# Optimization experiments

Hardware: AMD Instinct MI355X
Metric: run time of the kernel (lower is better)

Reference implementation:

```python
import jax, jax.numpy as jnp
import numpy as np

B, S, DIM, HEADS, DH = 1, 192, 512, 8, 64
LN_EPS = 1e-5


def setup_inputs() -> dict:
    key = jax.random.key(0)
    ks = jax.random.split(key, 5)
    rn = lambda k, shp: jax.random.normal(k, shp, dtype=jnp.float32) * 0.02
    return {
        "x": jax.random.normal(ks[0], (B, S, DIM), dtype=jnp.float32),
        "ln_w": jnp.ones((DIM,), jnp.float32),
        "ln_b": jnp.zeros((DIM,), jnp.float32),
        "W_abcde": rn(ks[1], (5 * HEADS * DH, DIM)),
        "b_abcde": jnp.zeros((5 * HEADS * DH,), jnp.float32),
        "W_K": rn(ks[2], (HEADS, DH, DH, DH)),
        "W_V": rn(ks[3], (HEADS, DH, DH, DH)),
        "W_out": rn(ks[4], (DIM, HEADS * DH)),
        "b_out": jnp.zeros((DIM,), jnp.float32),
    }


def reference(x, ln_w, ln_b, W_abcde, b_abcde, W_K, W_V, W_out, b_out):
    b, n, _ = x.shape
    # LayerNorm (biased variance, eps=1e-5, affine)
    mu = jnp.mean(x, axis=-1, keepdims=True)
    var = jnp.var(x, axis=-1, keepdims=True)
    xn = (x - mu) / jnp.sqrt(var + LN_EPS) * ln_w + ln_b
    # abcde projection, chunk into 5, split heads -> [b, n, h, d]
    proj = xn @ W_abcde.T + b_abcde
    a_, b_, c_, d_, e_ = [t.reshape(b, n, HEADS, DH) for t in jnp.split(proj, 5, axis=-1)]
    # cubic attention score chain (note: heads summed out in step2, reintroduced by a_)
    step1 = jnp.einsum('brnk,nijk->brij', c_, W_K)          # [b, r, d, d]
    step2 = jnp.einsum('brij,bqnj->briq', step1, b_)        # [b, r, d, q] (sum over heads of b_)
    attn = jnp.einsum('briq,bpni->bnpqr', step2, a_)        # [b, h, p, q, r]
    # "causal" mask: positions where p >= q set to 1e-6 (faithful to masked_fill_)
    t_idx = jnp.arange(n)[:, None, None]
    s_idx = jnp.arange(n)[None, :, None]
    mask = (t_idx >= s_idx)[None, None]                      # [1,1,p,q,1]
    attn = jnp.where(mask, jnp.float32(1e-6), attn)
    # 'b n p1 p2 p3 -> b n p3 (p1 p2)', scale by 1/dim_head, softmax over (p1 p2)
    attn = attn.transpose(0, 1, 4, 2, 3).reshape(b, HEADS, n, n * n) / DH
    attn = jax.nn.softmax(attn, axis=-1)
    # pairwise values: [b, p1, p2, h, d] -> 'b p s n h -> b n h (p s)'
    v = jnp.einsum('bpnh,bqng,nhgf->bpqnf', d_, e_, W_V)
    v = v.transpose(0, 3, 4, 1, 2).reshape(b, HEADS, DH, n * n)
    # weighted sum over pair axis, merge heads
    z = jnp.einsum('bnql,bnhl->bqnh', attn, v).reshape(b, n, HEADS * DH)
    return z @ W_out.T + b_out
```

## Files before the change

### kernel.cpp

```cpp
#include <hip/hip_runtime.h>
#include <hip/hip_bf16.h>
#include <cstdint>

#define SEQ 192

typedef float f32x4 __attribute__((ext_vector_type(4)));
typedef float f32x8 __attribute__((ext_vector_type(8)));
typedef __bf16 bf16;
typedef __bf16 bf16x8 __attribute__((ext_vector_type(8)));
typedef __bf16 bf16x4 __attribute__((ext_vector_type(4)));

#define MFMA_BF16(a, b, c) __builtin_amdgcn_mfma_f32_16x16x32_bf16(a, b, c, 0, 0, 0)

__device__ __forceinline__ bf16x8 cvt8(f32x8 v) {
  bf16x8 o;
#pragma unroll
  for (int i = 0; i < 8; i++) o[i] = (bf16)v[i];
  return o;
}

__global__ __launch_bounds__(256) void k1_prep(
    const float* __restrict__ x, const float* __restrict__ ln_w, const float* __restrict__ ln_b,
    const float* __restrict__ WV, bf16* __restrict__ xn_bf, bf16* __restrict__ WVt2) {
  int bid = blockIdx.x, tid = threadIdx.x;
  if (bid < 512) {
    int g = bid & 63, hh = bid >> 6;
    __shared__ float ld[64 * 65];
    int f = tid & 63, r4 = tid >> 6;
#pragma unroll
    for (int it = 0; it < 16; it++) {
      int hp = it * 4 + r4;
      ld[hp * 65 + f] = WV[(((size_t)(hh * 64 + hp) * 64 + g) * 64) + f];
    }
    __syncthreads();
    int hp2 = tid & 63;
#pragma unroll
    for (int it = 0; it < 16; it++) {
      int ff = it * 4 + r4;
      WVt2[(size_t)hh * 262144 + (size_t)(ff * 64 + g) * 64 + hp2] = (bf16)ld[hp2 * 65 + ff];
    }
    return;
  }
  bid -= 512;
  {
    int r = bid;
    const float* xr = x + (size_t)r * 512;
    float v0 = xr[tid], v1 = xr[tid + 256];
    float s = v0 + v1, s2 = v0 * v0 + v1 * v1;
#pragma unroll
    for (int off = 32; off > 0; off >>= 1) {
      s += __shfl_down(s, off);
      s2 += __shfl_down(s2, off);
    }
    __shared__ float redS[4], redS2[4];
    int wave = tid >> 6, lane = tid & 63;
    if (lane == 0) { redS[wave] = s; redS2[wave] = s2; }
    __syncthreads();
    float S = redS[0] + redS[1] + redS[2] + redS[3];
    float S2 = redS2[0] + redS2[1] + redS2[2] + redS2[3];
    float mean = S * (1.0f / 512.0f);
    float var = S2 * (1.0f / 512.0f) - mean * mean;
    float rstd = rsqrtf(var + 1e-5f);
    bf16* xnr = xn_bf + (size_t)r * 512;
    xnr[tid] = (bf16)((v0 - mean) * rstd * ln_w[tid] + ln_b[tid]);
    xnr[tid + 256] = (bf16)((v1 - mean) * rstd * ln_w[tid + 256] + ln_b[tid + 256]);
  }
}

template <int MODE>
__device__ __forceinline__ void gemm_body(const bf16* __restrict__ A, const bf16* __restrict__ Bt,
                                          bf16* __restrict__ C1, int N, int K,
                                          int nb, int mb, int tid) {
  int n0 = nb * 64, m0 = mb * 64;
  int wave = tid >> 6, lane = tid & 63;
  int lq = lane >> 4, l16 = lane & 15;
  const bf16* Ap = A + (size_t)(m0 + wave * 16 + l16) * K;
  f32x4 acc[4];
#pragma unroll
  for (int nt = 0; nt < 4; nt++) acc[nt] = (f32x4){0.f, 0.f, 0.f, 0.f};
  for (int k0 = 0; k0 < K; k0 += 32) {
    bf16x8 af = *(const bf16x8*)(Ap + k0 + lq * 8);
#pragma unroll
    for (int nt = 0; nt < 4; nt++) {
      bf16x8 bv = *(const bf16x8*)(Bt + (size_t)(n0 + nt * 16 + l16) * K + k0 + lq * 8);
      acc[nt] = MFMA_BF16(af, bv, acc[nt]);
    }
  }
  int cm = m0 + wave * 16 + lq * 4;
#pragma unroll
  for (int nt = 0; nt < 4; nt++) {
    int n = n0 + nt * 16 + l16;
    if constexpr (MODE == 1) {
#pragma unroll
      for (int rg = 0; rg < 4; rg++) C1[(size_t)(cm + rg) * N + n] = (bf16)acc[nt][rg];
    } else {
      int r = cm >> 6, i0 = cm & 63;
      bf16x4 pk = {(bf16)acc[nt][0], (bf16)acc[nt][1], (bf16)acc[nt][2], (bf16)acc[nt][3]};
      *(bf16x4*)(C1 + (size_t)r * 12288 + (size_t)n * 64 + i0) = pk;
    }
  }
}

__global__ __launch_bounds__(256) void k2_proj(
    const bf16* __restrict__ xn_bf, const float* __restrict__ Wab,
    const float* __restrict__ b_abcde, float* __restrict__ proj, bf16* __restrict__ a_bf,
    bf16* __restrict__ c_bf, bf16* __restrict__ d_bf) {
  int bid = blockIdx.x, tid = threadIdx.x;
  int nb = bid % 40, mb = bid / 40;
  int n0 = nb * 64, m0 = mb * 64;
  int wave = tid >> 6, lane = tid & 63;
  int lq = lane >> 4, l16 = lane & 15;
  const bf16* Ap = xn_bf + (size_t)(m0 + wave * 16 + l16) * 512;
  f32x4 acc[4];
#pragma unroll
  for (int nt = 0; nt < 4; nt++) acc[nt] = (f32x4){0.f, 0.f, 0.f, 0.f};
  for (int k0 = 0; k0 < 512; k0 += 32) {
    bf16x8 af = *(const bf16x8*)(Ap + k0 + lq * 8);
#pragma unroll
    for (int nt = 0; nt < 4; nt++) {
      f32x8 wv = *(const f32x8*)(Wab + (size_t)(n0 + nt * 16 + l16) * 512 + k0 + lq * 8);
      acc[nt] = MFMA_BF16(af, cvt8(wv), acc[nt]);
    }
  }
  int cm = m0 + wave * 16 + lq * 4;
#pragma unroll
  for (int nt = 0; nt < 4; nt++) {
    int n = n0 + nt * 16 + l16;
    int chunk = n >> 9, hcol = (n >> 6) & 7, i = n & 63;
#pragma unroll
    for (int rg = 0; rg < 4; rg++) {
      int m = cm + rg;
      float v = acc[nt][rg] + b_abcde[n];
      proj[(size_t)m * 2560 + n] = v;
      bf16 bv = (bf16)v;
      if (chunk == 0) a_bf[((size_t)hcol * SEQ + m) * 64 + i] = bv;
      else if (chunk == 2) c_bf[(size_t)m * 512 + (n - 1024)] = bv;
      else if (chunk == 3) d_bf[((size_t)hcol * SEQ + m) * 64 + i] = bv;
    }
  }
}

__global__ __launch_bounds__(256) void k3_mid(
    const bf16* __restrict__ c_bf, const float* __restrict__ WK, bf16* __restrict__ s1bf,
    const bf16* __restrict__ d_bf, const bf16* __restrict__ WVt2, bf16* __restrict__ tTt,
    const float* __restrict__ proj, bf16* __restrict__ eT_bf, float* __restrict__ ecum,
    bf16* __restrict__ bsum_bf) {
  __shared__ float el[64 * 65];
  int bid = blockIdx.x, tid = threadIdx.x;
  if (bid < 192) {
    int nb = bid % 64, mb = bid / 64;
    int n0 = nb * 64, m0 = mb * 64;
    int wave = tid >> 6, lane = tid & 63;
    int lq = lane >> 4, l16 = lane & 15;
    const bf16* Ap = c_bf + (size_t)(m0 + wave * 16 + l16) * 512;
    f32x4 acc[4];
#pragma unroll
    for (int nt = 0; nt < 4; nt++) acc[nt] = (f32x4){0.f, 0.f, 0.f, 0.f};
    size_t offn[4];
#pragma unroll
    for (int nt = 0; nt < 4; nt++) {
      int n = n0 + nt * 16 + l16;
      offn[nt] = (size_t)(n >> 6) * 4096 + (size_t)(n & 63) * 64;
    }
    for (int k0 = 0; k0 < 512; k0 += 32) {
      bf16x8 af = *(const bf16x8*)(Ap + k0 + lq * 8);
      size_t kb = (size_t)(k0 >> 6) * 262144 + (k0 & 32) + lq * 8;
#pragma unroll
      for (int nt = 0; nt < 4; nt++) {
        f32x8 wv = *(const f32x8*)(WK + kb + offn[nt]);
        acc[nt] = MFMA_BF16(af, cvt8(wv), acc[nt]);
      }
    }
    int cm = m0 + wave * 16 + lq * 4;
#pragma unroll
    for (int nt = 0; nt < 4; nt++) {
      int n = n0 + nt * 16 + l16;
#pragma unroll
      for (int rg = 0; rg < 4; rg++) s1bf[(size_t)(cm + rg) * 4096 + n] = (bf16)acc[nt][rg];
    }
    return;
  }
  bid -= 192;
  if (bid < 1536) {
    int h = bid / 192, rem = bid % 192;
    gemm_body<1>(d_bf + (size_t)h * 12288, WVt2 + (size_t)h * 262144,
                 tTt + (size_t)h * 786432, 4096, 64, rem % 64, rem / 64, tid);
    return;
  }
  bid -= 1536;
  if (bid < 8) {
    int h = bid;
    float carry = 0.f;
    for (int ch = 0; ch < 3; ch++) {
      int pbase = ch * 64;
      for (int idx = tid; idx < 4096; idx += 256) {
        int pl = idx >> 6, g = idx & 63;
        el[pl * 65 + g] = proj[(size_t)(pbase + pl) * 2560 + 2048 + h * 64 + g];
      }
      __syncthreads();
      for (int idx = tid; idx < 4096; idx += 256) {
        int g = idx >> 6, ql = idx & 63;
        eT_bf[((size_t)h * 64 + g) * SEQ + pbase + ql] = (bf16)el[ql * 65 + g];
      }
      if (tid < 64) {
        float run = carry;
        for (int pl = 0; pl < 64; pl++) {
          run += el[pl * 65 + tid];
          ecum[(size_t)h * 12288 + (pbase + pl) * 64 + tid] = run;
        }
        carry = run;
      }
      __syncthreads();
    }
    return;
  }
  bid -= 8;
  {
    int j = tid & 63, qg = tid >> 6;
#pragma unroll
    for (int qi = 0; qi < 16; qi++) {
      int q = bid * 64 + qg * 16 + qi;
      float s = 0.f;
#pragma unroll
      for (int hh = 0; hh < 8; hh++) s += proj[(size_t)q * 2560 + 512 + hh * 64 + j];
      bsum_bf[q * 64 + j] = (bf16)s;
    }
  }
}

__global__ __launch_bounds__(256) void k4_step2(const bf16* __restrict__ s1bf,
                                                const bf16* __restrict__ bsum_bf,
                                                bf16* __restrict__ s2bf) {
  int bid = blockIdx.x;
  gemm_body<2>(s1bf, bsum_bf, s2bf, 192, 64, bid % 3, bid / 3, threadIdx.x);
}

__global__ __launch_bounds__(256) void k5_attn(
    const bf16* __restrict__ a_bf, const bf16* __restrict__ s2bf,
    const bf16* __restrict__ eT_bf, const float* __restrict__ ecum,
    bf16* __restrict__ ew_bf, float* __restrict__ Lsum) {
  int r = blockIdx.x, h = blockIdx.y;
  int tid = threadIdx.x, wave = tid >> 6, lane = tid & 63;
  int lq = lane >> 4, l16 = lane & 15;
  __shared__ __align__(16) bf16 wch[4][16 * 40];
  __shared__ float redL[4];
  int pt[3] = {wave, wave + 4, 11 - wave};

  const bf16* ah = a_bf + (size_t)h * 12288;
  const bf16* s2r = s2bf + (size_t)r * 12288;
  const bf16* eh = eT_bf + (size_t)h * 12288;
  const float* ech = ecum + (size_t)h * 12288;
  bf16* myw = &wch[wave][0];

  bf16x8 afr[3][2];
#pragma unroll
  for (int mt = 0; mt < 3; mt++)
#pragma unroll
    for (int kc = 0; kc < 2; kc++)
      afr[mt][kc] = *(const bf16x8*)(ah + (pt[mt] * 16 + l16) * 64 + kc * 32 + lq * 8);

  f32x4 ewacc[3][4];
#pragma unroll
  for (int mt = 0; mt < 3; mt++)
#pragma unroll
    for (int nt = 0; nt < 4; nt++) ewacc[mt][nt] = (f32x4){0.f, 0.f, 0.f, 0.f};
  float lpart = 0.f;

  for (int c = 0; c < 6; c++) {
    if (c * 32 + 31 <= wave * 16) continue;
    bf16x8 efr[4];
#pragma unroll
    for (int nt = 0; nt < 4; nt++)
      efr[nt] = *(const bf16x8*)(eh + (nt * 16 + l16) * SEQ + c * 32 + lq * 8);
    bf16x8 bq0[2], bq1[2];
#pragma unroll
    for (int sub = 0; sub < 2; sub++) {
      int q = c * 32 + sub * 16 + l16;
      bq0[sub] = *(const bf16x8*)(s2r + q * 64 + lq * 8);
      bq1[sub] = *(const bf16x8*)(s2r + q * 64 + 32 + lq * 8);
    }
#pragma unroll
    for (int mt = 0; mt < 3; mt++) {
      int ptile = pt[mt];
      if (c * 32 + 31 <= ptile * 16) continue;
#pragma unroll
      for (int sub = 0; sub < 2; sub++) {
        if (c * 32 + sub * 16 + 15 <= ptile * 16) {
#pragma unroll
          for (int rg = 0; rg < 4; rg++) myw[(lq * 4 + rg) * 40 + sub * 16 + l16] = (bf16)0.f;
          continue;
        }
        f32x4 sv = (f32x4){0.f, 0.f, 0.f, 0.f};
        sv = MFMA_BF16(afr[mt][0], bq0[sub], sv);
        sv = MFMA_BF16(afr[mt][1], bq1[sub], sv);
        int q = c * 32 + sub * 16 + l16;
        int p0 = ptile * 16 + lq * 4;
#pragma unroll
        for (int rg = 0; rg < 4; rg++) {
          float wv = (q > p0 + rg) ? __expf(sv[rg] * 0.015625f) : 0.f;
          lpart += wv;
          myw[(lq * 4 + rg) * 40 + sub * 16 + l16] = (bf16)wv;
        }
      }
      bf16x8 wf = *(const bf16x8*)(myw + l16 * 40 + lq * 8);
#pragma unroll
      for (int nt = 0; nt < 4; nt++) ewacc[mt][nt] = MFMA_BF16(wf, efr[nt], ewacc[mt][nt]);
    }
  }

  bf16* ewout = ew_bf + ((size_t)h * SEQ + r) * 12288;
#pragma unroll
  for (int mt = 0; mt < 3; mt++)
#pragma unroll
    for (int nt = 0; nt < 4; nt++)
#pragma unroll
      for (int rg = 0; rg < 4; rg++) {
        int p = pt[mt] * 16 + lq * 4 + rg;
        int g = nt * 16 + l16;
        ewout[p * 64 + g] = (bf16)(ewacc[mt][nt][rg] + ech[p * 64 + g]);
      }

#pragma unroll
  for (int off = 32; off > 0; off >>= 1) lpart += __shfl_down(lpart, off);
  if (lane == 0) redL[wave] = lpart;
  __syncthreads();
  if (tid == 0) Lsum[h * SEQ + r] = redL[0] + redL[1] + redL[2] + redL[3];
}

__global__ __launch_bounds__(512) void k5b_z(
    const bf16* __restrict__ ew_bf, const bf16* __restrict__ tTt, float* __restrict__ Zpart) {
  int h = blockIdx.x, mt = blockIdx.y, ks = blockIdx.z;
  int tid = threadIdx.x, wave = tid >> 6, lane = tid & 63;
  int lq = lane >> 4, l16 = lane & 15;
  __shared__ float zred[8][16][66];
  const bf16* ewh = ew_bf + ((size_t)h * SEQ + mt * 16) * 12288;
  const bf16* th = tTt + (size_t)h * 786432;
  f32x4 acc[4];
#pragma unroll
  for (int nt = 0; nt < 4; nt++) acc[nt] = (f32x4){0.f, 0.f, 0.f, 0.f};
  for (int jj = 0; jj < 12; jj++) {
    int kc = ks * 96 + wave * 12 + jj;
    int p = kc >> 1, g0 = (kc & 1) * 32;
    bf16x8 af = *(const bf16x8*)(ewh + (size_t)l16 * 12288 + kc * 32 + lq * 8);
#pragma unroll
    for (int nt = 0; nt < 4; nt++) {
      bf16x8 tf = *(const bf16x8*)(th + (size_t)p * 4096 + (nt * 16 + l16) * 64 + g0 + lq * 8);
      acc[nt] = MFMA_BF16(af, tf, acc[nt]);
    }
  }
#pragma unroll
  for (int nt = 0; nt < 4; nt++)
#pragma unroll
    for (int rg = 0; rg < 4; rg++) zred[wave][lq * 4 + rg][nt * 16 + l16] = acc[nt][rg];
  __syncthreads();
#pragma unroll
  for (int o = 0; o < 2; o++) {
    int idx = o * 512 + tid;
    int rloc = idx >> 6, f = idx & 63;
    float s = 0.f;
#pragma unroll
    for (int wv = 0; wv < 8; wv++) s += zred[wv][rloc][f];
    Zpart[(size_t)ks * 98304 + (size_t)(mt * 16 + rloc) * 512 + h * 64 + f] = s;
  }
}

__global__ __launch_bounds__(256) void k6_out(
    const float* __restrict__ Zpart, const float* __restrict__ Lsum,
    const float* __restrict__ Wout, const float* __restrict__ b_out, float* __restrict__ out) {
  int bid = blockIdx.x, tid = threadIdx.x;
  int nb = bid & 7, mb = bid >> 3;
  int n0 = nb * 64, m0 = mb * 64;
  int wave = tid >> 6, lane = tid & 63;
  int lq = lane >> 4, l16 = lane & 15;
  int m = m0 + wave * 16 + l16;
  f32x4 acc[4];
#pragma unroll
  for (int nt = 0; nt < 4; nt++) acc[nt] = (f32x4){0.f, 0.f, 0.f, 0.f};
  for (int k0 = 0; k0 < 512; k0 += 32) {
    int h = k0 >> 6;
    float L = Lsum[h * SEQ + m] + 18528.0f;
    float rL = 1.0f / L;
    size_t zo = (size_t)m * 512 + k0 + lq * 8;
    f32x8 s = *(const f32x8*)(Zpart + zo);
    s += *(const f32x8*)(Zpart + 98304 + zo);
    s += *(const f32x8*)(Zpart + 196608 + zo);
    s += *(const f32x8*)(Zpart + 294912 + zo);
    bf16x8 af = cvt8(s * rL);
#pragma unroll
    for (int nt = 0; nt < 4; nt++) {
      f32x8 wv = *(const f32x8*)(Wout + (size_t)(n0 + nt * 16 + l16) * 512 + k0 + lq * 8);
      acc[nt] = MFMA_BF16(af, cvt8(wv), acc[nt]);
    }
  }
  int cm = m0 + wave * 16 + lq * 4;
#pragma unroll
  for (int nt = 0; nt < 4; nt++) {
    int n = n0 + nt * 16 + l16;
    float bv = b_out[n];
#pragma unroll
    for (int rg = 0; rg < 4; rg++) out[(size_t)(cm + rg) * 512 + n] = acc[nt][rg] + bv;
  }
}

static const size_t OFF_PROJ = 0;
static const size_t OFF_ECUM = 491520;
static const size_t OFF_XN = 589824;
static const size_t OFF_ZPART = 638976;
static const size_t OFF_LSUM = 1032192;
static const size_t OFF_WVT = 2473984;
static const size_t OFF_A = 3522560;
static const size_t OFF_C = 3571712;
static const size_t OFF_D = 3620864;
static const size_t OFF_ET = 3670016;
static const size_t OFF_BSUM = 3719168;
static const size_t OFF_S1 = 3725312;
static const size_t OFF_S2 = 4118528;
static const size_t OFF_TT = 5298176;
static const size_t OFF_EW = 8493056;

extern "C" void kernel_launch(void* const* d_in, const int* in_sizes, int n_in,
                              void* d_out, int out_size, void* d_ws, size_t ws_size,
                              hipStream_t stream) {
  (void)in_sizes; (void)n_in; (void)out_size; (void)ws_size;
  const float* x = (const float*)d_in[0];
  const float* ln_w = (const float*)d_in[1];
  const float* ln_b = (const float*)d_in[2];
  const float* W_abcde = (const float*)d_in[3];
  const float* b_abcde = (const float*)d_in[4];
  const float* W_K = (const float*)d_in[5];
  const float* W_V = (const float*)d_in[6];
  const float* W_out = (const float*)d_in[7];
  const float* b_out = (const float*)d_in[8];
  float* out = (float*)d_out;
  float* ws = (float*)d_ws;

  float* proj = ws + OFF_PROJ;
  float* ecum = ws + OFF_ECUM;
  bf16* xn_bf = (bf16*)(ws + OFF_XN);
  float* Zpart = ws + OFF_ZPART;
  float* Lsum = ws + OFF_LSUM;
  bf16* WVt2 = (bf16*)(ws + OFF_WVT);
  bf16* a_bf = (bf16*)(ws + OFF_A);
  bf16* c_bf = (bf16*)(ws + OFF_C);
  bf16* d_bf = (bf16*)(ws + OFF_D);
  bf16* eT_bf = (bf16*)(ws + OFF_ET);
  bf16* bsum_bf = (bf16*)(ws + OFF_BSUM);
  bf16* s1bf = (bf16*)(ws + OFF_S1);
  bf16* s2bf = (bf16*)(ws + OFF_S2);
  bf16* tTt = (bf16*)(ws + OFF_TT);
  bf16* ew_bf = (bf16*)(ws + OFF_EW);

  k1_prep<<<704, 256, 0, stream>>>(x, ln_w, ln_b, W_V, xn_bf, WVt2);
  k2_proj<<<120, 256, 0, stream>>>(xn_bf, W_abcde, b_abcde, proj, a_bf, c_bf, d_bf);
  k3_mid<<<1739, 256, 0, stream>>>(c_bf, W_K, s1bf, d_bf, WVt2, tTt, proj, eT_bf, ecum,
                                   bsum_bf);
  k4_step2<<<576, 256, 0, stream>>>(s1bf, bsum_bf, s2bf);
  k5_attn<<<dim3(SEQ, 8), 256, 0, stream>>>(a_bf, s2bf, eT_bf, ecum, ew_bf, Lsum);
  k5b_z<<<dim3(8, 12, 4), 512, 0, stream>>>(ew_bf, tTt, Zpart);
  k6_out<<<24, 256, 0, stream>>>(Zpart, Lsum, W_out, b_out, out);
}
```

Measured before the change: 255.5 us.

## Batch score MFMAs in attention kernel and retile Z reduction over more K splits

In k5_attn, all score MFMAs for the three p-tiles are now issued before the exp and LDS staging, and the per-wave staging buffer is split per tile and double-buffered by chunk parity. The goal is more independent MFMA work and fewer read-after-write stalls, paid for with more LDS and a launch bound of three blocks. k5b_z now computes two 16-row M tiles per block so each B fragment is reused twice, and the K split grows from 4 to 8 to keep the grid size the same. k6_out sums eight partials instead of four, and the Lsum offset moves to make room for the larger Zpart buffer.

```diff
diff --git a/kernel.cpp b/kernel.cpp
--- a/kernel.cpp
+++ b/kernel.cpp
@@ -235,14 +235,14 @@
   gemm_body<2>(s1bf, bsum_bf, s2bf, 192, 64, bid % 3, bid / 3, threadIdx.x);
 }
 
-__global__ __launch_bounds__(256) void k5_attn(
+__global__ __launch_bounds__(256, 3) void k5_attn(
     const bf16* __restrict__ a_bf, const bf16* __restrict__ s2bf,
     const bf16* __restrict__ eT_bf, const float* __restrict__ ecum,
     bf16* __restrict__ ew_bf, float* __restrict__ Lsum) {
   int r = blockIdx.x, h = blockIdx.y;
   int tid = threadIdx.x, wave = tid >> 6, lane = tid & 63;
   int lq = lane >> 4, l16 = lane & 15;
-  __shared__ __align__(16) bf16 wch[4][16 * 40];
+  __shared__ __align__(16) bf16 wch[2][4][3][16 * 40];
   __shared__ float redL[4];
   int pt[3] = {wave, wave + 4, 11 - wave};
 
@@ -250,7 +250,6 @@
   const bf16* s2r = s2bf + (size_t)r * 12288;
   const bf16* eh = eT_bf + (size_t)h * 12288;
   const float* ech = ecum + (size_t)h * 12288;
-  bf16* myw = &wch[wave][0];
 
   bf16x8 afr[3][2];
 #pragma unroll
@@ -268,41 +267,55 @@
 
   for (int c = 0; c < 6; c++) {
     if (c * 32 + 31 <= wave * 16) continue;
+    int par = c & 1;
     bf16x8 efr[4];
 #pragma unroll
     for (int nt = 0; nt < 4; nt++)
       efr[nt] = *(const bf16x8*)(eh + (nt * 16 + l16) * SEQ + c * 32 + lq * 8);
-    bf16x8 bq0[2], bq1[2];
+    bf16x8 bq[2][2];
 #pragma unroll
     for (int sub = 0; sub < 2; sub++) {
       int q = c * 32 + sub * 16 + l16;
-      bq0[sub] = *(const bf16x8*)(s2r + q * 64 + lq * 8);
-      bq1[sub] = *(const bf16x8*)(s2r + q * 64 + 32 + lq * 8);
-    }
+      bq[sub][0] = *(const bf16x8*)(s2r + q * 64 + lq * 8);
+      bq[sub][1] = *(const bf16x8*)(s2r + q * 64 + 32 + lq * 8);
+    }
+    f32x4 sacc[3][2];
 #pragma unroll
     for (int mt = 0; mt < 3; mt++) {
-      int ptile = pt[mt];
-      if (c * 32 + 31 <= ptile * 16) continue;
+      if (c * 32 + 31 <= pt[mt] * 16) continue;
 #pragma unroll
       for (int sub = 0; sub < 2; sub++) {
-        if (c * 32 + sub * 16 + 15 <= ptile * 16) {
-#pragma unroll
-          for (int rg = 0; rg < 4; rg++) myw[(lq * 4 + rg) * 40 + sub * 16 + l16] = (bf16)0.f;
+        if (c * 32 + sub * 16 + 15 <= pt[mt] * 16) continue;
+        f32x4 sv = (f32x4){0.f, 0.f, 0.f, 0.f};
+        sv = MFMA_BF16(afr[mt][0], bq[sub][0], sv);
+        sacc[mt][sub] = MFMA_BF16(afr[mt][1], bq[sub][1], sv);
+      }
+    }
+#pragma unroll
+    for (int mt = 0; mt < 3; mt++) {
+      if (c * 32 + 31 <= pt[mt] * 16) continue;
+      bf16* mybuf = &wch[par][wave][mt][0];
+#pragma unroll
+      for (int sub = 0; sub < 2; sub++) {
+        if (c * 32 + sub * 16 + 15 <= pt[mt] * 16) {
+#pragma unroll
+          for (int rg = 0; rg < 4; rg++) mybuf[(lq * 4 + rg) * 40 + sub * 16 + l16] = (bf16)0.f;
           continue;
         }
-        f32x4 sv = (f32x4){0.f, 0.f, 0.f, 0.f};
-        sv = MFMA_BF16(afr[mt][0], bq0[sub], sv);
-        sv = MFMA_BF16(afr[mt][1], bq1[sub], sv);
         int q = c * 32 + sub * 16 + l16;
-        int p0 = ptile * 16 + lq * 4;
+        int p0 = pt[mt] * 16 + lq * 4;
 #pragma unroll
         for (int rg = 0; rg < 4; rg++) {
-          float wv = (q > p0 + rg) ? __expf(sv[rg] * 0.015625f) : 0.f;
+          float wv = (q > p0 + rg) ? __expf(sacc[mt][sub][rg] * 0.015625f) : 0.f;
           lpart += wv;
-          myw[(lq * 4 + rg) * 40 + sub * 16 + l16] = (bf16)wv;
+          mybuf[(lq * 4 + rg) * 40 + sub * 16 + l16] = (bf16)wv;
         }
       }
-      bf16x8 wf = *(const bf16x8*)(myw + l16 * 40 + lq * 8);
+    }
+#pragma unroll
+    for (int mt = 0; mt < 3; mt++) {
+      if (c * 32 + 31 <= pt[mt] * 16) continue;
+      bf16x8 wf = *(const bf16x8*)(&wch[par][wave][mt][l16 * 40 + lq * 8]);
 #pragma unroll
       for (int nt = 0; nt < 4; nt++) ewacc[mt][nt] = MFMA_BF16(wf, efr[nt], ewacc[mt][nt]);
     }
@@ -333,34 +346,42 @@
   int tid = threadIdx.x, wave = tid >> 6, lane = tid & 63;
   int lq = lane >> 4, l16 = lane & 15;
   __shared__ float zred[8][16][66];
-  const bf16* ewh = ew_bf + ((size_t)h * SEQ + mt * 16) * 12288;
+  const bf16* ewh = ew_bf + ((size_t)h * SEQ + mt * 32) * 12288;
   const bf16* th = tTt + (size_t)h * 786432;
-  f32x4 acc[4];
-#pragma unroll
-  for (int nt = 0; nt < 4; nt++) acc[nt] = (f32x4){0.f, 0.f, 0.f, 0.f};
-  for (int jj = 0; jj < 12; jj++) {
-    int kc = ks * 96 + wave * 12 + jj;
+  f32x4 acc[2][4];
+#pragma unroll
+  for (int m2 = 0; m2 < 2; m2++)
+#pragma unroll
+    for (int nt = 0; nt < 4; nt++) acc[m2][nt] = (f32x4){0.f, 0.f, 0.f, 0.f};
+  for (int jj = 0; jj < 6; jj++) {
+    int kc = ks * 48 + wave * 6 + jj;
     int p = kc >> 1, g0 = (kc & 1) * 32;
-    bf16x8 af = *(const bf16x8*)(ewh + (size_t)l16 * 12288 + kc * 32 + lq * 8);
+    bf16x8 af0 = *(const bf16x8*)(ewh + (size_t)l16 * 12288 + kc * 32 + lq * 8);
+    bf16x8 af1 = *(const bf16x8*)(ewh + (size_t)(16 + l16) * 12288 + kc * 32 + lq * 8);
 #pragma unroll
     for (int nt = 0; nt < 4; nt++) {
       bf16x8 tf = *(const bf16x8*)(th + (size_t)p * 4096 + (nt * 16 + l16) * 64 + g0 + lq * 8);
-      acc[nt] = MFMA_BF16(af, tf, acc[nt]);
-    }
-  }
-#pragma unroll
-  for (int nt = 0; nt < 4; nt++)
-#pragma unroll
-    for (int rg = 0; rg < 4; rg++) zred[wave][lq * 4 + rg][nt * 16 + l16] = acc[nt][rg];
-  __syncthreads();
-#pragma unroll
-  for (int o = 0; o < 2; o++) {
-    int idx = o * 512 + tid;
-    int rloc = idx >> 6, f = idx & 63;
-    float s = 0.f;
-#pragma unroll
-    for (int wv = 0; wv < 8; wv++) s += zred[wv][rloc][f];
-    Zpart[(size_t)ks * 98304 + (size_t)(mt * 16 + rloc) * 512 + h * 64 + f] = s;
+      acc[0][nt] = MFMA_BF16(af0, tf, acc[0][nt]);
+      acc[1][nt] = MFMA_BF16(af1, tf, acc[1][nt]);
+    }
+  }
+#pragma unroll
+  for (int m2 = 0; m2 < 2; m2++) {
+    if (m2) __syncthreads();
+#pragma unroll
+    for (int nt = 0; nt < 4; nt++)
+#pragma unroll
+      for (int rg = 0; rg < 4; rg++) zred[wave][lq * 4 + rg][nt * 16 + l16] = acc[m2][nt][rg];
+    __syncthreads();
+#pragma unroll
+    for (int o = 0; o < 2; o++) {
+      int idx = o * 512 + tid;
+      int rloc = idx >> 6, f = idx & 63;
+      float s = 0.f;
+#pragma unroll
+      for (int wv = 0; wv < 8; wv++) s += zred[wv][rloc][f];
+      Zpart[(size_t)ks * 98304 + (size_t)(mt * 32 + m2 * 16 + rloc) * 512 + h * 64 + f] = s;
+    }
   }
 }
 
@@ -382,9 +403,8 @@
     float rL = 1.0f / L;
     size_t zo = (size_t)m * 512 + k0 + lq * 8;
     f32x8 s = *(const f32x8*)(Zpart + zo);
-    s += *(const f32x8*)(Zpart + 98304 + zo);
-    s += *(const f32x8*)(Zpart + 196608 + zo);
-    s += *(const f32x8*)(Zpart + 294912 + zo);
+#pragma unroll
+    for (int ks = 1; ks < 8; ks++) s += *(const f32x8*)(Zpart + (size_t)ks * 98304 + zo);
     bf16x8 af = cvt8(s * rL);
 #pragma unroll
     for (int nt = 0; nt < 4; nt++) {
@@ -406,7 +426,7 @@
 static const size_t OFF_ECUM = 491520;
 static const size_t OFF_XN = 589824;
 static const size_t OFF_ZPART = 638976;
-static const size_t OFF_LSUM = 1032192;
+static const size_t OFF_LSUM = 1425408;
 static const size_t OFF_WVT = 2473984;
 static const size_t OFF_A = 3522560;
 static const size_t OFF_C = 3571712;
@@ -456,6 +476,6 @@
                                    bsum_bf);
   k4_step2<<<576, 256, 0, stream>>>(s1bf, bsum_bf, s2bf);
   k5_attn<<<dim3(SEQ, 8), 256, 0, stream>>>(a_bf, s2bf, eT_bf, ecum, ew_bf, Lsum);
-  k5b_z<<<dim3(8, 12, 4), 512, 0, stream>>>(ew_bf, tTt, Zpart);
+  k5b_z<<<dim3(8, 6, 8), 512, 0, stream>>>(ew_bf, tTt, Zpart);
   k6_out<<<24, 256, 0, stream>>>(Zpart, Lsum, W_out, b_out, out);
 }
```

New measurement: 255.8 us. About the same (+0.1%).
